# Performance work log

Measured on AMD Instinct MI355X. Metric: run time of the kernel, lower is better.

Reference implementation:

```python
import jax, jax.numpy as jnp
import numpy as np

N = 100000        # vertices
E = 20000         # hyperedges
NNZ = 1000000     # incidence pairs
IN_CH = 128
HEADS = 8
OUT_CH = 16
D = HEADS * OUT_CH  # 128
NUM_TYPES = 16
K_CURV = 1.0      # Lorentz k = 1/c with c = 1


def lorentz_linear(x, W, b, scale_log):
    # HyboNet LorentzLinear: linear map, then project onto hyperboloid.
    y = x @ W.T + b                                   # [N, D]
    time = jax.nn.sigmoid(y[..., :1]) * jnp.exp(scale_log) + 1.1  # [N, 1]
    x_narrow = y[..., 1:]                             # [N, D-1]
    sq = jnp.sum(x_narrow * x_narrow, axis=-1, keepdims=True)
    scale = (time * time - K_CURV) / (sq + 1e-8)
    return jnp.concatenate([time, x_narrow * jnp.sqrt(scale)], axis=-1)


def setup_inputs() -> dict:
    key = jax.random.key(0)
    ks = jax.random.split(key, 8)
    X = jax.random.normal(ks[0], (N, IN_CH), dtype=jnp.float32)
    emb_ty = jax.random.normal(ks[1], (NUM_TYPES, D), dtype=jnp.float32)
    vertex = jax.random.randint(ks[2], (NNZ,), 0, N, dtype=jnp.int32)
    edges = jax.random.randint(ks[3], (NNZ,), 0, E, dtype=jnp.int32)
    type_ids = jax.random.randint(ks[4], (NNZ,), 0, NUM_TYPES, dtype=jnp.int32)
    # LorentzLinear params (nn.Linear with bias, scale init log(10))
    W = jax.random.normal(ks[5], (D, IN_CH), dtype=jnp.float32) / np.sqrt(IN_CH)
    b = jnp.zeros((D,), dtype=jnp.float32)
    scale_log = jnp.asarray(np.log(10.0), dtype=jnp.float32)
    eps = jnp.asarray([0.5], dtype=jnp.float32)
    return {"X": X, "emb_ty": emb_ty, "W": W, "b": b, "scale_log": scale_log,
            "eps": eps, "vertex": vertex, "edges": edges, "type_ids": type_ids,
            "num_edges": E}


def reference(X, emb_ty, W, b, scale_log, eps, vertex, edges, type_ids, num_edges):
    n = X.shape[0]
    Xh = lorentz_linear(X, W, b, scale_log)           # [N, D]
    Xve = Xh[vertex] - emb_ty[type_ids]               # [NNZ, D] gather + subtract
    Xe = jax.ops.segment_sum(Xve, edges, num_segments=num_edges)  # [E, D]
    Xev = Xe[edges]                                   # [NNZ, D]
    Xv = jax.ops.segment_sum(Xev, vertex, num_segments=n)         # [N, D]
    return eps * Xv + Xh
```

## Files before the change

### kernel.cpp

```cpp
#include <hip/hip_runtime.h>
#include <hip/hip_bf16.h>


#define E_SEGS 20000

__global__ __launch_bounds__(256) void lorentz_gemm_kernel(
    const float* __restrict__ X, const float* __restrict__ W,
    const float* __restrict__ bias, const float* __restrict__ scale_log,
    float* __restrict__ Xh, int N)
{
    __shared__ float4 Ws[128 * 9];
    __shared__ float4 Xs[64 * 9];
    const int t = threadIdx.x;
    const int row0 = blockIdx.x * 64;

    const int rg = t >> 4;
    const int cg = t & 15;
    const int sr = t >> 3;
    const int sc = t & 7;

    float acc[4][8];
    #pragma unroll
    for (int r = 0; r < 4; ++r)
        #pragma unroll
        for (int j = 0; j < 8; ++j) acc[r][j] = 0.f;

    for (int ch = 0; ch < 4; ++ch) {
        if (ch) __syncthreads();
        const int kb = ch * 8;
        #pragma unroll
        for (int i = 0; i < 4; ++i) {
            int d = sr + i * 32;
            Ws[d * 9 + (sc ^ ((d >> 3) & 7))] =
                ((const float4*)W)[(size_t)d * 32 + kb + sc];
        }
        #pragma unroll
        for (int i = 0; i < 2; ++i) {
            int r = sr + i * 32;
            int gr = row0 + r;
            float4 x = make_float4(0.f, 0.f, 0.f, 0.f);
            if (gr < N) x = ((const float4*)X)[(size_t)gr * 32 + kb + sc];
            Xs[r * 9 + sc] = x;
        }
        __syncthreads();

        #pragma unroll
        for (int k4 = 0; k4 < 8; ++k4) {
            float4 xq[4];
            #pragma unroll
            for (int rr = 0; rr < 4; ++rr)
                xq[rr] = Xs[(rg * 4 + rr) * 9 + k4];
            float4 wq[8];
            const int wc = k4 ^ (cg & 7);
            #pragma unroll
            for (int j = 0; j < 8; ++j)
                wq[j] = Ws[(cg * 8 + j) * 9 + wc];
            #pragma unroll
            for (int rr = 0; rr < 4; ++rr)
                #pragma unroll
                for (int j = 0; j < 8; ++j)
                    acc[rr][j] += xq[rr].x * wq[j].x + xq[rr].y * wq[j].y
                                + xq[rr].z * wq[j].z + xq[rr].w * wq[j].w;
        }
    }

    const int cb = cg << 3;
    float4 b0 = ((const float4*)bias)[cg * 2];
    float4 b1 = ((const float4*)bias)[cg * 2 + 1];
    #pragma unroll
    for (int r = 0; r < 4; ++r) {
        acc[r][0] += b0.x; acc[r][1] += b0.y; acc[r][2] += b0.z; acc[r][3] += b0.w;
        acc[r][4] += b1.x; acc[r][5] += b1.y; acc[r][6] += b1.z; acc[r][7] += b1.w;
    }

    const float es = expf(scale_log[0]);

    #pragma unroll
    for (int r = 0; r < 4; ++r) {
        float sq = 0.f;
        #pragma unroll
        for (int j = 0; j < 8; ++j) sq += acc[r][j] * acc[r][j];
        if (cg == 0) sq -= acc[r][0] * acc[r][0];
        #pragma unroll
        for (int m = 1; m < 16; m <<= 1) sq += __shfl_xor(sq, m, 16);
        float y0   = __shfl(acc[r][0], 0, 16);
        float time = es / (1.f + expf(-y0)) + 1.1f;
        float ss   = sqrtf((time * time - 1.f) / (sq + 1e-8f));
        float4 o0, o1;
        o0.x = (cg == 0) ? time : acc[r][0] * ss;
        o0.y = acc[r][1] * ss; o0.z = acc[r][2] * ss; o0.w = acc[r][3] * ss;
        o1.x = acc[r][4] * ss; o1.y = acc[r][5] * ss;
        o1.z = acc[r][6] * ss; o1.w = acc[r][7] * ss;
        int grow = row0 + (rg << 2) + r;
        if (grow < N) {
            float4* ph = (float4*)(Xh + (size_t)grow * 128 + cb);
            ph[0] = o0; ph[1] = o1;
        }
    }
}

__global__ __launch_bounds__(256) void count_both_kernel(
    const int* __restrict__ edges, const int* __restrict__ vertex,
    int* __restrict__ hist_e, int* __restrict__ hist_v, int n)
{
    int i = blockIdx.x * 256 + threadIdx.x;
    if (i < n) {
        atomicAdd(&hist_e[edges[i]], 1);
        atomicAdd(&hist_v[vertex[i]], 1);
    }
}

__global__ __launch_bounds__(256) void scan_partial_kernel(
    const int* __restrict__ counts, int* __restrict__ offs,
    int* __restrict__ bsums, int n)
{
    __shared__ int buf[256];
    const int b = blockIdx.x, tid = threadIdx.x;
    const int i0 = b * 1024 + tid * 4;
    int c0 = (i0 + 0 < n) ? counts[i0 + 0] : 0;
    int c1 = (i0 + 1 < n) ? counts[i0 + 1] : 0;
    int c2 = (i0 + 2 < n) ? counts[i0 + 2] : 0;
    int c3 = (i0 + 3 < n) ? counts[i0 + 3] : 0;
    int s = c0 + c1 + c2 + c3;
    buf[tid] = s;
    __syncthreads();
    #pragma unroll
    for (int off = 1; off < 256; off <<= 1) {
        int v = (tid >= off) ? buf[tid - off] : 0;
        __syncthreads();
        buf[tid] += v;
        __syncthreads();
    }
    int ex = buf[tid] - s;
    if (i0 + 0 < n) offs[i0 + 0] = ex;
    if (i0 + 1 < n) offs[i0 + 1] = ex + c0;
    if (i0 + 2 < n) offs[i0 + 2] = ex + c0 + c1;
    if (i0 + 3 < n) offs[i0 + 3] = ex + c0 + c1 + c2;
    if (tid == 255) bsums[b] = buf[255];
}

__global__ __launch_bounds__(256) void scan_bsums_kernel(
    int* __restrict__ bsums, int nb)
{
    __shared__ int buf[256];
    const int tid = threadIdx.x;
    int v = (tid < nb) ? bsums[tid] : 0;
    buf[tid] = v;
    __syncthreads();
    #pragma unroll
    for (int off = 1; off < 256; off <<= 1) {
        int u = (tid >= off) ? buf[tid - off] : 0;
        __syncthreads();
        buf[tid] += u;
        __syncthreads();
    }
    if (tid < nb) bsums[tid] = buf[tid] - v;
}

__global__ __launch_bounds__(256) void scan_add_kernel(
    int* __restrict__ offs, const int* __restrict__ bsums, int n, int total)
{
    const int b = blockIdx.x, tid = threadIdx.x;
    const int add = bsums[b];
    const int i0 = b * 1024 + tid * 4;
    if (add != 0) {
        if (i0 + 0 < n) offs[i0 + 0] += add;
        if (i0 + 1 < n) offs[i0 + 1] += add;
        if (i0 + 2 < n) offs[i0 + 2] += add;
        if (i0 + 3 < n) offs[i0 + 3] += add;
    }
    if (b == 0 && tid == 0) offs[n] = total;
}

__global__ __launch_bounds__(256) void fill_both_kernel(
    const int* __restrict__ edges, const int* __restrict__ vertex,
    const int* __restrict__ types,
    int* __restrict__ cur_e, int* __restrict__ vals_e,
    int* __restrict__ cur_v, int* __restrict__ segs_v, int n)
{
    int i = blockIdx.x * 256 + threadIdx.x;
    if (i < n) {
        int s = edges[i];
        int v = vertex[i];
        int pe = atomicAdd(&cur_e[s], 1);
        vals_e[pe] = v | (types[i] << 17);
        int pv = atomicAdd(&cur_v[v], 1);
        segs_v[pv] = s;
    }
}

__global__ __launch_bounds__(256) void edge_gather_kernel(
    const float* __restrict__ Xh, const float* __restrict__ emb,
    const int* __restrict__ offs, const int* __restrict__ vals,
    float* __restrict__ Xe, int nsegs)
{
    int seg = blockIdx.x * 4 + (threadIdx.x >> 6);
    if (seg >= nsegs) return;
    const int lane = threadIdx.x & 63;
    const int h = lane >> 5, l5 = lane & 31;
    const int beg = offs[seg], end = offs[seg + 1];
    float4 acc = make_float4(0.f, 0.f, 0.f, 0.f);
    for (int e = beg + h; e < end; e += 2) {
        int p  = vals[e];
        int v  = p & 0x1FFFF, ty = p >> 17;
        float4 a = ((const float4*)Xh)[(size_t)v * 32 + l5];
        float4 m = ((const float4*)emb)[ty * 32 + l5];
        acc.x += a.x - m.x; acc.y += a.y - m.y;
        acc.z += a.z - m.z; acc.w += a.w - m.w;
    }
    acc.x += __shfl_xor(acc.x, 32);
    acc.y += __shfl_xor(acc.y, 32);
    acc.z += __shfl_xor(acc.z, 32);
    acc.w += __shfl_xor(acc.w, 32);
    if (h == 0) ((float4*)Xe)[(size_t)seg * 32 + l5] = acc;
}

__global__ __launch_bounds__(256) void vertex_gather_kernel(
    const float* __restrict__ Xh, const float* __restrict__ Xe,
    const int* __restrict__ offs, const int* __restrict__ segs,
    const float* __restrict__ eps, float* __restrict__ out, int N)
{
    int v = blockIdx.x * 4 + (threadIdx.x >> 6);
    if (v >= N) return;
    const int lane = threadIdx.x & 63;
    const int h = lane >> 5, l5 = lane & 31;
    const int beg = offs[v], end = offs[v + 1];
    float4 acc = make_float4(0.f, 0.f, 0.f, 0.f);
    for (int e = beg + h; e < end; e += 2) {
        int s = segs[e];
        float4 a = ((const float4*)Xe)[(size_t)s * 32 + l5];
        acc.x += a.x; acc.y += a.y; acc.z += a.z; acc.w += a.w;
    }
    acc.x += __shfl_xor(acc.x, 32);
    acc.y += __shfl_xor(acc.y, 32);
    acc.z += __shfl_xor(acc.z, 32);
    acc.w += __shfl_xor(acc.w, 32);
    if (h == 0) {
        float ep = eps[0];
        float4 xh = ((const float4*)Xh)[(size_t)v * 32 + l5];
        float4 o;
        o.x = xh.x + ep * acc.x; o.y = xh.y + ep * acc.y;
        o.z = xh.z + ep * acc.z; o.w = xh.w + ep * acc.w;
        ((float4*)out)[(size_t)v * 32 + l5] = o;
    }
}

extern "C" void kernel_launch(void* const* d_in, const int* in_sizes, int n_in,
                              void* d_out, int out_size, void* d_ws, size_t ws_size,
                              hipStream_t stream) {
    const float* X         = (const float*)d_in[0];
    const float* emb_ty    = (const float*)d_in[1];
    const float* W         = (const float*)d_in[2];
    const float* bias      = (const float*)d_in[3];
    const float* scale_log = (const float*)d_in[4];
    const float* eps       = (const float*)d_in[5];
    const int*   vertex    = (const int*)d_in[6];
    const int*   edges     = (const int*)d_in[7];
    const int*   type_ids  = (const int*)d_in[8];

    const int N   = in_sizes[0] / 128;
    const int nnz = in_sizes[6];
    const int E   = E_SEGS;

    float* Xh = (float*)d_ws;
    float* Xe = Xh + (size_t)N * 128;
    int* ip      = (int*)(Xe + (size_t)E * 128);
    int* offs_e  = ip;              ip += E + 1;
    int* offs_v  = ip;              ip += N + 1;
    int* hist_e  = ip;              ip += E;
    int* hist_v  = ip;              ip += N;
    int* cur_e   = ip;              ip += E;
    int* cur_v   = ip;              ip += N;
    int* bsum_e  = ip;              ip += 256;
    int* bsum_v  = ip;              ip += 256;
    int* vals_e  = ip;              ip += nnz;
    int* segs_v  = ip;              ip += nnz;

    hipMemsetAsync(hist_e, 0, (size_t)(E + N) * sizeof(int), stream);

    float* out = (float*)d_out;
    const int blocks_nnz = (nnz + 255) / 256;
    const int nb_e = (E + 1023) / 1024;
    const int nb_v = (N + 1023) / 1024;

    count_both_kernel<<<blocks_nnz, 256, 0, stream>>>(
        edges, vertex, hist_e, hist_v, nnz);

    scan_partial_kernel<<<nb_e, 256, 0, stream>>>(hist_e, offs_e, bsum_e, E);
    scan_partial_kernel<<<nb_v, 256, 0, stream>>>(hist_v, offs_v, bsum_v, N);
    scan_bsums_kernel<<<1, 256, 0, stream>>>(bsum_e, nb_e);
    scan_bsums_kernel<<<1, 256, 0, stream>>>(bsum_v, nb_v);
    scan_add_kernel<<<nb_e, 256, 0, stream>>>(offs_e, bsum_e, E, nnz);
    scan_add_kernel<<<nb_v, 256, 0, stream>>>(offs_v, bsum_v, N, nnz);

    hipMemcpyAsync(cur_e, offs_e, (size_t)E * sizeof(int),
                   hipMemcpyDeviceToDevice, stream);
    hipMemcpyAsync(cur_v, offs_v, (size_t)N * sizeof(int),
                   hipMemcpyDeviceToDevice, stream);
    fill_both_kernel<<<blocks_nnz, 256, 0, stream>>>(
        edges, vertex, type_ids, cur_e, vals_e, cur_v, segs_v, nnz);

    lorentz_gemm_kernel<<<(N + 63) / 64, 256, 0, stream>>>(
        X, W, bias, scale_log, Xh, N);

    edge_gather_kernel<<<(E + 3) / 4, 256, 0, stream>>>(
        Xh, emb_ty, offs_e, vals_e, Xe, E);

    vertex_gather_kernel<<<(N + 3) / 4, 256, 0, stream>>>(
        Xh, Xe, offs_v, segs_v, eps, out, N);
}
```

Before: 657.2 us.

## Replace random-atomic CSR fill with two-level bucketed scatter

```diff
diff --git a/kernel.cpp b/kernel.cpp
--- a/kernel.cpp
+++ b/kernel.cpp
@@ -3,6 +3,8 @@
 
 
 #define E_SEGS 20000
+#define NBKT_MAX 128
+#define CHUNK 4096
 
 __global__ __launch_bounds__(256) void lorentz_gemm_kernel(
     const float* __restrict__ X, const float* __restrict__ W,
@@ -172,20 +174,95 @@
     if (b == 0 && tid == 0) offs[n] = total;
 }
 
-__global__ __launch_bounds__(256) void fill_both_kernel(
+__global__ __launch_bounds__(256) void init_bcur_kernel(
+    const int* __restrict__ offs_e, const int* __restrict__ offs_v,
+    int* __restrict__ bcur_e, int* __restrict__ bcur_v,
+    int shift_e, int ne, int shift_v, int nv)
+{
+    int b = threadIdx.x;
+    if (b < NBKT_MAX) {
+        int ke = b << shift_e; if (ke > ne) ke = ne;
+        bcur_e[b] = offs_e[ke];
+        int kv = b << shift_v; if (kv > nv) kv = nv;
+        bcur_v[b] = offs_v[kv];
+    }
+}
+
+__global__ __launch_bounds__(256) void bucket_scatter_kernel(
     const int* __restrict__ edges, const int* __restrict__ vertex,
-    const int* __restrict__ types,
-    int* __restrict__ cur_e, int* __restrict__ vals_e,
-    int* __restrict__ cur_v, int* __restrict__ segs_v, int n)
-{
-    int i = blockIdx.x * 256 + threadIdx.x;
-    if (i < n) {
-        int s = edges[i];
-        int v = vertex[i];
-        int pe = atomicAdd(&cur_e[s], 1);
-        vals_e[pe] = v | (types[i] << 17);
-        int pv = atomicAdd(&cur_v[v], 1);
-        segs_v[pv] = s;
+    const int* __restrict__ types, int mode, int shift,
+    int* __restrict__ bcur, int2* __restrict__ P, int n)
+{
+    __shared__ int hist[NBKT_MAX];
+    __shared__ int lstart[NBKT_MAX];
+    __shared__ int gbase[NBKT_MAX];
+    __shared__ int cur2[NBKT_MAX];
+    __shared__ int s_tot;
+    __shared__ int2 stage[CHUNK];
+    const int tid = threadIdx.x;
+    const int c0 = blockIdx.x * CHUNK;
+
+    for (int j = tid; j < NBKT_MAX; j += 256) hist[j] = 0;
+    __syncthreads();
+
+    int myk[16], myp[16];
+    #pragma unroll
+    for (int u = 0; u < 16; ++u) {
+        int i = c0 + tid + u * 256;
+        int k = -1, p = 0;
+        if (i < n) {
+            if (mode == 0) { k = edges[i];  p = vertex[i] | (types[i] << 17); }
+            else           { k = vertex[i]; p = edges[i]; }
+        }
+        myk[u] = k; myp[u] = p;
+        if (k >= 0) atomicAdd(&hist[k >> shift], 1);
+    }
+    __syncthreads();
+
+    if (tid == 0) {
+        int run = 0;
+        #pragma unroll 4
+        for (int b = 0; b < NBKT_MAX; ++b) { lstart[b] = run; run += hist[b]; }
+        s_tot = run;
+    }
+    __syncthreads();
+    if (tid < NBKT_MAX) {
+        cur2[tid] = lstart[tid];
+        int h = hist[tid];
+        gbase[tid] = h ? atomicAdd(&bcur[tid], h) : 0;
+    }
+    __syncthreads();
+
+    #pragma unroll
+    for (int u = 0; u < 16; ++u) {
+        int k = myk[u];
+        if (k >= 0) {
+            int pos = atomicAdd(&cur2[k >> shift], 1);
+            stage[pos] = make_int2(k, myp[u]);
+        }
+    }
+    __syncthreads();
+
+    const int tot = s_tot;
+    for (int j = tid; j < tot; j += 256) {
+        int2 e = stage[j];
+        int b = e.x >> shift;
+        P[gbase[b] + (j - lstart[b])] = e;
+    }
+}
+
+__global__ __launch_bounds__(256) void bucket_place_kernel(
+    const int2* __restrict__ P, const int* __restrict__ offs,
+    int* __restrict__ cur, int* __restrict__ dst, int shift, int nkeys)
+{
+    const int b = blockIdx.x;
+    int klo = b << shift;
+    int khi = klo + (1 << shift); if (khi > nkeys) khi = nkeys;
+    const int beg = offs[klo], end = offs[khi];
+    for (int j = beg + (int)threadIdx.x; j < end; j += 256) {
+        int2 e = P[j];
+        int pos = atomicAdd(&cur[e.x], 1);
+        dst[pos] = e.y;
     }
 }
 
@@ -262,6 +339,11 @@
     const int nnz = in_sizes[6];
     const int E   = E_SEGS;
 
+    const int shift_e = 8;
+    const int shift_v = 10;
+    const int nb_bkt_e = (E + 255) >> 8;
+    const int nb_bkt_v = (N + 1023) >> 10;
+
     float* Xh = (float*)d_ws;
     float* Xe = Xh + (size_t)N * 128;
     int* ip      = (int*)(Xe + (size_t)E * 128);
@@ -273,13 +355,19 @@
     int* cur_v   = ip;              ip += N;
     int* bsum_e  = ip;              ip += 256;
     int* bsum_v  = ip;              ip += 256;
+    int* bcur_e  = ip;              ip += NBKT_MAX;
+    int* bcur_v  = ip;              ip += NBKT_MAX;
     int* vals_e  = ip;              ip += nnz;
     int* segs_v  = ip;              ip += nnz;
 
+    int2* P_e = (int2*)Xh;
+    int2* P_v = P_e + nnz;
+
     hipMemsetAsync(hist_e, 0, (size_t)(E + N) * sizeof(int), stream);
 
     float* out = (float*)d_out;
     const int blocks_nnz = (nnz + 255) / 256;
+    const int blocks_chk = (nnz + CHUNK - 1) / CHUNK;
     const int nb_e = (E + 1023) / 1024;
     const int nb_v = (N + 1023) / 1024;
 
@@ -293,12 +381,20 @@
     scan_add_kernel<<<nb_e, 256, 0, stream>>>(offs_e, bsum_e, E, nnz);
     scan_add_kernel<<<nb_v, 256, 0, stream>>>(offs_v, bsum_v, N, nnz);
 
+    init_bcur_kernel<<<1, 256, 0, stream>>>(
+        offs_e, offs_v, bcur_e, bcur_v, shift_e, E, shift_v, N);
     hipMemcpyAsync(cur_e, offs_e, (size_t)E * sizeof(int),
                    hipMemcpyDeviceToDevice, stream);
     hipMemcpyAsync(cur_v, offs_v, (size_t)N * sizeof(int),
                    hipMemcpyDeviceToDevice, stream);
-    fill_both_kernel<<<blocks_nnz, 256, 0, stream>>>(
-        edges, vertex, type_ids, cur_e, vals_e, cur_v, segs_v, nnz);
+    bucket_scatter_kernel<<<blocks_chk, 256, 0, stream>>>(
+        edges, vertex, type_ids, 0, shift_e, bcur_e, P_e, nnz);
+    bucket_scatter_kernel<<<blocks_chk, 256, 0, stream>>>(
+        edges, vertex, type_ids, 1, shift_v, bcur_v, P_v, nnz);
+    bucket_place_kernel<<<nb_bkt_e, 256, 0, stream>>>(
+        P_e, offs_e, cur_e, vals_e, shift_e, E);
+    bucket_place_kernel<<<nb_bkt_v, 256, 0, stream>>>(
+        P_v, offs_v, cur_v, segs_v, shift_v, N);
 
     lorentz_gemm_kernel<<<(N + 63) / 64, 256, 0, stream>>>(
         X, W, bias, scale_log, Xh, N);
```

After: 616.7 us. 1.07x faster.
